# Optimization experiments

Hardware: AMD Instinct MI355X
Metric: run time of the kernel (lower is better)

The kernel has to match this reference:

```python
import jax, jax.numpy as jnp
import numpy as np

EPS = 1e-4


def setup_inputs() -> dict:
    key = jax.random.key(0)
    ks = jax.random.split(key, 16)
    N, D, H, K = 262144, 162, 256, 30
    s = 0.05  # weight init scale
    return {
        "Yh": jax.random.uniform(ks[0], (N, D), dtype=jnp.float32),
        "u": jax.random.uniform(ks[1], (1,), dtype=jnp.float32),
        "W1": jax.random.normal(ks[2], (D, H), dtype=jnp.float32) * s,
        "b1": jnp.zeros((H,), jnp.float32),
        "W2": jax.random.normal(ks[3], (H, H), dtype=jnp.float32) * s,
        "b2": jnp.zeros((H,), jnp.float32),
        "Wa": jax.random.normal(ks[4], (H, K), dtype=jnp.float32) * s,
        "ba": jnp.zeros((K,), jnp.float32),
        "Wb": jax.random.normal(ks[5], (H, K), dtype=jnp.float32) * s,
        "bb": jnp.zeros((K,), jnp.float32),
        "Wd1": jax.random.normal(ks[6], (K, H), dtype=jnp.float32) * s,
        "bd1": jnp.zeros((H,), jnp.float32),
        "Wd2": jax.random.normal(ks[7], (H, D), dtype=jnp.float32) * s,
        "bd2": jnp.zeros((D,), jnp.float32),
    }


def _stick_segments(v):
    # pi_k = v_k * prod_{j<k} (1 - v_j)  (vectorized exclusive cumprod,
    # replacing the original per-dim Python loop)
    cp = jnp.cumprod(1.0 - v, axis=1)  # [N, K]
    excl = jnp.concatenate([jnp.ones_like(v[:, :1]), cp[:, :-1]], axis=1)
    return v * excl


def reference(Yh, u, W1, b1, W2, b2, Wa, ba, Wb, bb, Wd1, bd1, Wd2, bd2):
    # encode_hsi: dense MLP -> positive Kumaraswamy params (softplus heads)
    h = jax.nn.relu(Yh @ W1 + b1)
    h = jax.nn.relu(h @ W2 + b2)
    alpha = jax.nn.softplus(h @ Wa + ba) + EPS  # param1_hsi [N, K]
    beta = jax.nn.softplus(h @ Wb + bb) + EPS   # param2_hsi [N, K]
    # Kumaraswamy reparametrization with a single shared uniform sample
    uu = u[0] * 0.98 + 0.01  # Uniform(0.01, 0.99) scalar
    v = (1.0 - uu ** (1.0 / beta)) ** (1.0 / alpha)  # [N, K]
    # set_v_K_to_one: force last stick proportion to 1
    v = jnp.concatenate([v[:, :-1], jnp.ones_like(v[:, :1])], axis=1)
    pi_h = _stick_segments(v)  # [N, K], rows sum to 1
    # decode: MLP -> sigmoid (positive outputs, recon.log() finite)
    d = jax.nn.relu(pi_h @ Wd1 + bd1)
    recon = jax.nn.sigmoid(d @ Wd2 + bd2)  # [N, D]
    return recon, alpha, beta, pi_h
```

## Files before the change

### kernel.cpp

```cpp
#include <hip/hip_runtime.h>
#include <hip/hip_bf16.h>

#define N_ROWS 262144
#define D_IN 162
#define K_DIM 30
#define ROWS 32

using bf16_t = __hip_bfloat16;
typedef __attribute__((ext_vector_type(8))) short bf16x8;
typedef __attribute__((ext_vector_type(4))) float f32x4;

__device__ __forceinline__ int swz_byte(int row, int col) {
  int b = (row << 9) + (col << 1);
  return b ^ ((row & 7) << 4);
}

__device__ __forceinline__ uint32_t bf16b(float x) {
  return (uint32_t)__builtin_bit_cast(unsigned short, __float2bfloat16(x));
}
__device__ __forceinline__ uint32_t pack2(float lo, float hi) {
  return bf16b(lo) | (bf16b(hi) << 16);
}
__device__ __forceinline__ float unpk_lo(uint32_t p) {
  return __bfloat162float(__builtin_bit_cast(__hip_bfloat16, (unsigned short)(p & 0xffff)));
}
__device__ __forceinline__ float unpk_hi(uint32_t p) {
  return __bfloat162float(__builtin_bit_cast(__hip_bfloat16, (unsigned short)(p >> 16)));
}
__device__ __forceinline__ float softplus_f(float x) {
  return (x > 15.f) ? x : log1pf(__expf(x));
}

__global__ void pack_b_kernel(const float* __restrict__ src, bf16_t* __restrict__ dst,
                              int K, int N, int Np, int KB) {
  int idx = blockIdx.x * 256 + threadIdx.x;
  int total = KB * Np * 32;
  if (idx >= total) return;
  int ks = idx & 31;
  int n  = (idx >> 5) % Np;
  int kb = idx / (32 * Np);
  int k  = kb * 32 + ks;
  float v = (k < K && n < N) ? src[k * N + n] : 0.f;
  dst[idx] = __float2bfloat16(v);
}

__global__ void pack_ab_kernel(const float* __restrict__ Wa, const float* __restrict__ Wb,
                               bf16_t* __restrict__ dst) {
  int idx = blockIdx.x * 256 + threadIdx.x;
  if (idx >= 8 * 64 * 32) return;
  int ks = idx & 31;
  int n  = (idx >> 5) & 63;
  int kb = idx >> 11;
  int k  = kb * 32 + ks;
  int j = n >> 1, s = n & 1;
  float v = (j < K_DIM) ? (s ? Wb[k * K_DIM + j] : Wa[k * K_DIM + j]) : 0.f;
  dst[idx] = __float2bfloat16(v);
}

template<int KB, int NP, int NMO>
__device__ __forceinline__ void gemm_acc(const uint8_t* lds, int srcOff,
                                         const bf16_t* __restrict__ Wp, int ocBase,
                                         int lr, int lg, f32x4 (&acc)[NMO][2]) {
  int bE[2], bO[2];
#pragma unroll
  for (int nr = 0; nr < 2; ++nr) {
    bE[nr] = srcOff + swz_byte(16 * nr + lr, 8 * lg);
    bO[nr] = srcOff + swz_byte(16 * nr + lr, 32 + 8 * lg);
  }
#pragma unroll
  for (int kb = 0; kb < KB; ++kb) {
    bf16x8 wf[NMO];
#pragma unroll
    for (int mo = 0; mo < NMO; ++mo)
      wf[mo] = *reinterpret_cast<const bf16x8*>(Wp + ((kb * NP + ocBase + 16 * mo + lr) << 5) + 8 * lg);
    bf16x8 hf[2];
#pragma unroll
    for (int nr = 0; nr < 2; ++nr) {
      int base = (kb & 1) ? bO[nr] : bE[nr];
      hf[nr] = *reinterpret_cast<const bf16x8*>(lds + base + (kb >> 1) * 128);
    }
#pragma unroll
    for (int mo = 0; mo < NMO; ++mo)
#pragma unroll
      for (int nr = 0; nr < 2; ++nr)
        acc[mo][nr] = __builtin_amdgcn_mfma_f32_16x16x32_bf16(wf[mo], hf[nr], acc[mo][nr], 0, 0, 0);
  }
}

template<int NMO>
__device__ __forceinline__ void acc_bias_init(const float* __restrict__ bias, int ocBase,
                                              int lg, f32x4 (&acc)[NMO][2]) {
#pragma unroll
  for (int mo = 0; mo < NMO; ++mo) {
    float4 bv = *reinterpret_cast<const float4*>(bias + ocBase + 16 * mo + 4 * lg);
    f32x4 t = {bv.x, bv.y, bv.z, bv.w};
#pragma unroll
    for (int nr = 0; nr < 2; ++nr) acc[mo][nr] = t;
  }
}

template<int NMO>
__device__ __forceinline__ void epi_relu_store(uint8_t* lds, int dstOff, int ocBase,
                                               int lr, int lg, f32x4 (&acc)[NMO][2]) {
#pragma unroll
  for (int mo = 0; mo < NMO; ++mo)
#pragma unroll
    for (int nr = 0; nr < 2; ++nr) {
      int row = 16 * nr + lr;
      int col = ocBase + 16 * mo + 4 * lg;
      float x0 = fmaxf(acc[mo][nr][0], 0.f), x1 = fmaxf(acc[mo][nr][1], 0.f);
      float x2 = fmaxf(acc[mo][nr][2], 0.f), x3 = fmaxf(acc[mo][nr][3], 0.f);
      uint2 p; p.x = pack2(x0, x1); p.y = pack2(x2, x3);
      *reinterpret_cast<uint2*>(lds + dstOff + swz_byte(row, col)) = p;
    }
}

#define OFF_H 16384
#define OFF_PI 8192
__launch_bounds__(256, 4)
__global__ void usdn_fused(const float* __restrict__ Yh, const float* __restrict__ u,
                           const float* __restrict__ b1, const float* __restrict__ b2,
                           const float* __restrict__ ba, const float* __restrict__ bb,
                           const float* __restrict__ bd1, const float* __restrict__ bd2,
                           const bf16_t* __restrict__ Wp1, const bf16_t* __restrict__ Wp2,
                           const bf16_t* __restrict__ Wpab, const bf16_t* __restrict__ Wpd1,
                           const bf16_t* __restrict__ Wpd2,
                           float* __restrict__ outRecon, float* __restrict__ outAlpha,
                           float* __restrict__ outBeta, float* __restrict__ outPi) {
  __shared__ __align__(16) uint8_t lds[32768];

  const int tid = threadIdx.x;
  const int w  = tid >> 6;
  const int l  = tid & 63;
  const int lr = l & 15;
  const int lg = l >> 4;
  const int r0 = blockIdx.x * ROWS;

  {
    int row = tid >> 3, l8 = tid & 7;
    const float2* src = reinterpret_cast<const float2*>(Yh + (size_t)(r0 + row) * D_IN);
#pragma unroll
    for (int it = 0; it < 12; ++it) {
      int f2 = l8 + it * 8;
      uint32_t p = 0;
      if (f2 < 81) { float2 v = src[f2]; p = pack2(v.x, v.y); }
      if (f2 < 96) *reinterpret_cast<uint32_t*>(lds + swz_byte(row, f2 * 2)) = p;
    }
  }
  __syncthreads();

  {
    f32x4 acc[4][2];
    acc_bias_init<4>(b1, w * 64, lg, acc);
    gemm_acc<6, 256, 4>(lds, 0, Wp1, w * 64, lr, lg, acc);
    epi_relu_store<4>(lds, OFF_H, w * 64, lr, lg, acc);
  }
  __syncthreads();

  {
    f32x4 acc[4][2];
    acc_bias_init<4>(b2, w * 64, lg, acc);
    gemm_acc<8, 256, 4>(lds, OFF_H, Wp2, w * 64, lr, lg, acc);
    __syncthreads();
    epi_relu_store<4>(lds, OFF_H, w * 64, lr, lg, acc);
  }
  __syncthreads();

  float regA0[2], regA1[2], regB0[2], regB1[2];
  int   j0 = 8 * w + 2 * lg;
  {
    bool jv = (j0 < K_DIM);
    float ba0 = jv ? ba[j0] : 0.f,     bb0 = jv ? bb[j0] : 0.f;
    float ba1 = jv ? ba[j0 + 1] : 0.f, bb1 = jv ? bb[j0 + 1] : 0.f;
    f32x4 acc[1][2];
    f32x4 binit = {ba0, bb0, ba1, bb1};
    acc[0][0] = binit; acc[0][1] = binit;
    gemm_acc<8, 64, 1>(lds, OFF_H, Wpab, 16 * w, lr, lg, acc);

    float uu  = u[0] * 0.98f + 0.01f;
    float l2u = log2f(uu);
    float* vbuf = reinterpret_cast<float*>(lds);
#pragma unroll
    for (int nr = 0; nr < 2; ++nr) {
      int row = 16 * nr + lr;
      float a0 = softplus_f(acc[0][nr][0]) + 1e-4f;
      float b0v = softplus_f(acc[0][nr][1]) + 1e-4f;
      float a1 = softplus_f(acc[0][nr][2]) + 1e-4f;
      float b1v = softplus_f(acc[0][nr][3]) + 1e-4f;
      regA0[nr] = a0; regB0[nr] = b0v; regA1[nr] = a1; regB1[nr] = b1v;
      if (jv) {
        if (j0 < K_DIM - 1) {
          float t = exp2f(l2u / b0v);
          vbuf[row * 33 + j0] = exp2f(log2f(1.f - t) / a0);
        }
        if (j0 + 1 < K_DIM - 1) {
          float t = exp2f(l2u / b1v);
          vbuf[row * 33 + j0 + 1] = exp2f(log2f(1.f - t) / a1);
        }
      }
    }
  }
  __syncthreads();

  if (tid < ROWS) {
    const float* vbuf = reinterpret_cast<const float*>(lds);
    bf16_t* piT = reinterpret_cast<bf16_t*>(lds + OFF_PI);
    int row = tid;
    float ex = 1.f;
#pragma unroll
    for (int j = 0; j < K_DIM - 1; ++j) {
      float vj = vbuf[row * 33 + j];
      float pi = vj * ex;
      piT[row * 40 + j] = __float2bfloat16(pi);
      ex *= (1.f - vj);
    }
    piT[row * 40 + (K_DIM - 1)] = __float2bfloat16(ex);
    piT[row * 40 + 30] = __float2bfloat16(0.f);
    piT[row * 40 + 31] = __float2bfloat16(0.f);
  }
  __syncthreads();

  {
    f32x4 acc[4][2];
    acc_bias_init<4>(bd1, w * 64, lg, acc);
    bf16x8 pf[2];
#pragma unroll
    for (int nr = 0; nr < 2; ++nr)
      pf[nr] = *reinterpret_cast<const bf16x8*>(lds + OFF_PI + (16 * nr + lr) * 80 + 16 * lg);
#pragma unroll
    for (int mo = 0; mo < 4; ++mo) {
      bf16x8 wf = *reinterpret_cast<const bf16x8*>(Wpd1 + ((w * 64 + 16 * mo + lr) << 5) + 8 * lg);
#pragma unroll
      for (int nr = 0; nr < 2; ++nr)
        acc[mo][nr] = __builtin_amdgcn_mfma_f32_16x16x32_bf16(wf, pf[nr], acc[mo][nr], 0, 0, 0);
    }
    epi_relu_store<4>(lds, OFF_H, w * 64, lr, lg, acc);
  }
  __syncthreads();

  {
    f32x4 acc[3][2];
#pragma unroll
    for (int mo = 0; mo < 3; ++mo) {
      int col0 = 48 * w + 16 * mo + 4 * lg;
      f32x4 t;
#pragma unroll
      for (int i = 0; i < 4; ++i) t[i] = (col0 + i < D_IN) ? bd2[col0 + i] : 0.f;
#pragma unroll
      for (int nr = 0; nr < 2; ++nr) acc[mo][nr] = t;
    }
    gemm_acc<8, 192, 3>(lds, OFF_H, Wpd2, 48 * w, lr, lg, acc);
#pragma unroll
    for (int mo = 0; mo < 3; ++mo) {
      int col0 = 48 * w + 16 * mo + 4 * lg;
#pragma unroll
      for (int nr = 0; nr < 2; ++nr) {
        int row = 16 * nr + lr;
        float s0 = 1.f / (1.f + __expf(-acc[mo][nr][0]));
        float s1 = 1.f / (1.f + __expf(-acc[mo][nr][1]));
        float s2 = 1.f / (1.f + __expf(-acc[mo][nr][2]));
        float s3 = 1.f / (1.f + __expf(-acc[mo][nr][3]));
        float* dst = outRecon + (size_t)(r0 + row) * D_IN + col0;
        if (col0 < D_IN)     *reinterpret_cast<float2*>(dst)     = make_float2(s0, s1);
        if (col0 + 2 < D_IN) *reinterpret_cast<float2*>(dst + 2) = make_float2(s2, s3);
      }
    }
  }

  if (j0 < K_DIM) {
#pragma unroll
    for (int nr = 0; nr < 2; ++nr) {
      int row = 16 * nr + lr;
      size_t base = (size_t)(r0 + row) * K_DIM + j0;
      *reinterpret_cast<float2*>(outAlpha + base) = make_float2(regA0[nr], regA1[nr]);
      *reinterpret_cast<float2*>(outBeta  + base) = make_float2(regB0[nr], regB1[nr]);
    }
  }
  {
    int row = tid >> 3, l8 = tid & 7;
#pragma unroll
    for (int half = 0; half < 2; ++half) {
      int f2 = l8 + half * 8;
      if (f2 < 15) {
        uint32_t pp = *reinterpret_cast<const uint32_t*>(lds + OFF_PI + row * 80 + f2 * 4);
        *reinterpret_cast<float2*>(outPi + (size_t)(r0 + row) * K_DIM + f2 * 2) =
            make_float2(unpk_lo(pp), unpk_hi(pp));
      }
    }
  }
}

extern "C" void kernel_launch(void* const* d_in, const int* in_sizes, int n_in,
                              void* d_out, int out_size, void* d_ws, size_t ws_size,
                              hipStream_t stream) {
  const float* Yh  = (const float*)d_in[0];
  const float* u   = (const float*)d_in[1];
  const float* W1  = (const float*)d_in[2];
  const float* b1  = (const float*)d_in[3];
  const float* W2  = (const float*)d_in[4];
  const float* b2  = (const float*)d_in[5];
  const float* Wa  = (const float*)d_in[6];
  const float* ba  = (const float*)d_in[7];
  const float* Wb  = (const float*)d_in[8];
  const float* bb  = (const float*)d_in[9];
  const float* Wd1 = (const float*)d_in[10];
  const float* bd1 = (const float*)d_in[11];
  const float* Wd2 = (const float*)d_in[12];
  const float* bd2 = (const float*)d_in[13];

  bf16_t* ws   = (bf16_t*)d_ws;
  bf16_t* Wp1  = ws;
  bf16_t* Wp2  = Wp1 + 49152;
  bf16_t* Wpab = Wp2 + 65536;
  bf16_t* Wpd1 = Wpab + 16384;
  bf16_t* Wpd2 = Wpd1 + 8192;

  float* outRecon = (float*)d_out;
  float* outAlpha = outRecon + (size_t)N_ROWS * D_IN;
  float* outBeta  = outAlpha + (size_t)N_ROWS * K_DIM;
  float* outPi    = outBeta  + (size_t)N_ROWS * K_DIM;

  pack_b_kernel<<<192, 256, 0, stream>>>(W1, Wp1, 162, 256, 256, 6);
  pack_b_kernel<<<256, 256, 0, stream>>>(W2, Wp2, 256, 256, 256, 8);
  pack_ab_kernel<<<64, 256, 0, stream>>>(Wa, Wb, Wpab);
  pack_b_kernel<<<32, 256, 0, stream>>>(Wd1, Wpd1, 30, 256, 256, 1);
  pack_b_kernel<<<192, 256, 0, stream>>>(Wd2, Wpd2, 256, 162, 192, 8);

  usdn_fused<<<N_ROWS / ROWS, 256, 0, stream>>>(Yh, u, b1, b2, ba, bb, bd1, bd2,
                                                Wp1, Wp2, Wpab, Wpd1, Wpd2,
                                                outRecon, outAlpha, outBeta, outPi);
}
```

Measured before the change: 280.7 us.

## Prefetch weight fragments across GEMM stages with double-buffered registers and ping-pong LDS

Weight fragments for each GEMM are now loaded two k-blocks ahead into a register double buffer, and the next stage's first fragments are issued before the current stage's epilogue. This is meant to hide global/L2 weight-load latency behind MFMA work. LDS buffers now alternate between two regions, which removes the intra-stage barrier before the layer-2 writeback. The cost is higher register pressure, which could cause spills or lower occupancy under launch_bounds(256,4).

```diff
diff --git a/kernel.cpp b/kernel.cpp
--- a/kernel.cpp
+++ b/kernel.cpp
@@ -57,10 +57,20 @@
   dst[idx] = __float2bfloat16(v);
 }
 
+template<int NP, int NMO>
+__device__ __forceinline__ void wload(const bf16_t* __restrict__ Wp, int kb, int ocBase,
+                                      int lr, int lg, bf16x8 (&out)[NMO]) {
+#pragma unroll
+  for (int mo = 0; mo < NMO; ++mo)
+    out[mo] = *reinterpret_cast<const bf16x8*>(
+        Wp + ((kb * NP + ocBase + 16 * mo + lr) << 5) + 8 * lg);
+}
+
 template<int KB, int NP, int NMO>
-__device__ __forceinline__ void gemm_acc(const uint8_t* lds, int srcOff,
-                                         const bf16_t* __restrict__ Wp, int ocBase,
-                                         int lr, int lg, f32x4 (&acc)[NMO][2]) {
+__device__ __forceinline__ void gemm_roll(const uint8_t* lds, int srcOff,
+                                          const bf16_t* __restrict__ Wp, int ocBase,
+                                          int lr, int lg, f32x4 (&acc)[NMO][2],
+                                          bf16x8 (&wbuf)[2][NMO]) {
   int bE[2], bO[2];
 #pragma unroll
   for (int nr = 0; nr < 2; ++nr) {
@@ -69,10 +79,11 @@
   }
 #pragma unroll
   for (int kb = 0; kb < KB; ++kb) {
-    bf16x8 wf[NMO];
-#pragma unroll
-    for (int mo = 0; mo < NMO; ++mo)
-      wf[mo] = *reinterpret_cast<const bf16x8*>(Wp + ((kb * NP + ocBase + 16 * mo + lr) << 5) + 8 * lg);
+    bf16x8 cur[NMO];
+#pragma unroll
+    for (int mo = 0; mo < NMO; ++mo) cur[mo] = wbuf[kb & 1][mo];
+    if (kb + 2 < KB)
+      wload<NP, NMO>(Wp, kb + 2, ocBase, lr, lg, wbuf[kb & 1]);
     bf16x8 hf[2];
 #pragma unroll
     for (int nr = 0; nr < 2; ++nr) {
@@ -83,7 +94,7 @@
     for (int mo = 0; mo < NMO; ++mo)
 #pragma unroll
       for (int nr = 0; nr < 2; ++nr)
-        acc[mo][nr] = __builtin_amdgcn_mfma_f32_16x16x32_bf16(wf[mo], hf[nr], acc[mo][nr], 0, 0, 0);
+        acc[mo][nr] = __builtin_amdgcn_mfma_f32_16x16x32_bf16(cur[mo], hf[nr], acc[mo][nr], 0, 0, 0);
   }
 }
 
@@ -115,8 +126,9 @@
     }
 }
 
-#define OFF_H 16384
-#define OFF_PI 8192
+#define OFF_B  16384
+#define OFF_PI (16384 + 8192)
+
 __launch_bounds__(256, 4)
 __global__ void usdn_fused(const float* __restrict__ Yh, const float* __restrict__ u,
                            const float* __restrict__ b1, const float* __restrict__ b2,
@@ -136,57 +148,93 @@
   const int lg = l >> 4;
   const int r0 = blockIdx.x * ROWS;
 
-  {
-    int row = tid >> 3, l8 = tid & 7;
-    const float2* src = reinterpret_cast<const float2*>(Yh + (size_t)(r0 + row) * D_IN);
+  const int srow = tid >> 3, sl8 = tid & 7;
+  float2 sv[12];
+  {
+    const float2* src = reinterpret_cast<const float2*>(Yh + (size_t)(r0 + srow) * D_IN);
 #pragma unroll
     for (int it = 0; it < 12; ++it) {
-      int f2 = l8 + it * 8;
+      int f2 = sl8 + it * 8;
+      if (f2 < 81) sv[it] = src[f2];
+    }
+  }
+  bf16x8 w1buf[2][4];
+  wload<256, 4>(Wp1, 0, w * 64, lr, lg, w1buf[0]);
+  wload<256, 4>(Wp1, 1, w * 64, lr, lg, w1buf[1]);
+  {
+#pragma unroll
+    for (int it = 0; it < 12; ++it) {
+      int f2 = sl8 + it * 8;
       uint32_t p = 0;
-      if (f2 < 81) { float2 v = src[f2]; p = pack2(v.x, v.y); }
-      if (f2 < 96) *reinterpret_cast<uint32_t*>(lds + swz_byte(row, f2 * 2)) = p;
-    }
-  }
-  __syncthreads();
-
+      if (f2 < 81) p = pack2(sv[it].x, sv[it].y);
+      if (f2 < 96) *reinterpret_cast<uint32_t*>(lds + swz_byte(srow, f2 * 2)) = p;
+    }
+  }
+  __syncthreads();
+
+  bf16x8 w2buf[2][4];
   {
     f32x4 acc[4][2];
     acc_bias_init<4>(b1, w * 64, lg, acc);
-    gemm_acc<6, 256, 4>(lds, 0, Wp1, w * 64, lr, lg, acc);
-    epi_relu_store<4>(lds, OFF_H, w * 64, lr, lg, acc);
-  }
-  __syncthreads();
-
+    gemm_roll<6, 256, 4>(lds, 0, Wp1, w * 64, lr, lg, acc, w1buf);
+    wload<256, 4>(Wp2, 0, w * 64, lr, lg, w2buf[0]);
+    wload<256, 4>(Wp2, 1, w * 64, lr, lg, w2buf[1]);
+    epi_relu_store<4>(lds, OFF_B, w * 64, lr, lg, acc);
+  }
+  __syncthreads();
+
+  bf16x8 wh[8];
   {
     f32x4 acc[4][2];
     acc_bias_init<4>(b2, w * 64, lg, acc);
-    gemm_acc<8, 256, 4>(lds, OFF_H, Wp2, w * 64, lr, lg, acc);
-    __syncthreads();
-    epi_relu_store<4>(lds, OFF_H, w * 64, lr, lg, acc);
+    gemm_roll<8, 256, 4>(lds, OFF_B, Wp2, w * 64, lr, lg, acc, w2buf);
+#pragma unroll
+    for (int kb = 0; kb < 8; ++kb)
+      wh[kb] = *reinterpret_cast<const bf16x8*>(Wpab + ((kb * 64 + 16 * w + lr) << 5) + 8 * lg);
+    epi_relu_store<4>(lds, 0, w * 64, lr, lg, acc);
   }
   __syncthreads();
 
   float regA0[2], regA1[2], regB0[2], regB1[2];
-  int   j0 = 8 * w + 2 * lg;
+  const int j0 = 8 * w + 2 * lg;
+  bf16x8 w4[4];
+  bf16x8 w5buf[2][3];
   {
     bool jv = (j0 < K_DIM);
     float ba0 = jv ? ba[j0] : 0.f,     bb0 = jv ? bb[j0] : 0.f;
     float ba1 = jv ? ba[j0 + 1] : 0.f, bb1 = jv ? bb[j0 + 1] : 0.f;
-    f32x4 acc[1][2];
+    f32x4 acc[2];
     f32x4 binit = {ba0, bb0, ba1, bb1};
-    acc[0][0] = binit; acc[0][1] = binit;
-    gemm_acc<8, 64, 1>(lds, OFF_H, Wpab, 16 * w, lr, lg, acc);
+    acc[0] = binit; acc[1] = binit;
+    int bE[2], bO[2];
+#pragma unroll
+    for (int nr = 0; nr < 2; ++nr) {
+      bE[nr] = swz_byte(16 * nr + lr, 8 * lg);
+      bO[nr] = swz_byte(16 * nr + lr, 32 + 8 * lg);
+    }
+#pragma unroll
+    for (int kb = 0; kb < 8; ++kb) {
+#pragma unroll
+      for (int nr = 0; nr < 2; ++nr) {
+        int base = (kb & 1) ? bO[nr] : bE[nr];
+        bf16x8 hf = *reinterpret_cast<const bf16x8*>(lds + base + (kb >> 1) * 128);
+        acc[nr] = __builtin_amdgcn_mfma_f32_16x16x32_bf16(wh[kb], hf, acc[nr], 0, 0, 0);
+      }
+    }
+    wload<256, 4>(Wpd1, 0, w * 64, lr, lg, w4);
+    wload<192, 3>(Wpd2, 0, 48 * w, lr, lg, w5buf[0]);
+    wload<192, 3>(Wpd2, 1, 48 * w, lr, lg, w5buf[1]);
 
     float uu  = u[0] * 0.98f + 0.01f;
     float l2u = log2f(uu);
-    float* vbuf = reinterpret_cast<float*>(lds);
+    float* vbuf = reinterpret_cast<float*>(lds + OFF_B);
 #pragma unroll
     for (int nr = 0; nr < 2; ++nr) {
       int row = 16 * nr + lr;
-      float a0 = softplus_f(acc[0][nr][0]) + 1e-4f;
-      float b0v = softplus_f(acc[0][nr][1]) + 1e-4f;
-      float a1 = softplus_f(acc[0][nr][2]) + 1e-4f;
-      float b1v = softplus_f(acc[0][nr][3]) + 1e-4f;
+      float a0  = softplus_f(acc[nr][0]) + 1e-4f;
+      float b0v = softplus_f(acc[nr][1]) + 1e-4f;
+      float a1  = softplus_f(acc[nr][2]) + 1e-4f;
+      float b1v = softplus_f(acc[nr][3]) + 1e-4f;
       regA0[nr] = a0; regB0[nr] = b0v; regA1[nr] = a1; regB1[nr] = b1v;
       if (jv) {
         if (j0 < K_DIM - 1) {
@@ -203,7 +251,7 @@
   __syncthreads();
 
   if (tid < ROWS) {
-    const float* vbuf = reinterpret_cast<const float*>(lds);
+    const float* vbuf = reinterpret_cast<const float*>(lds + OFF_B);
     bf16_t* piT = reinterpret_cast<bf16_t*>(lds + OFF_PI);
     int row = tid;
     float ex = 1.f;
@@ -228,13 +276,11 @@
     for (int nr = 0; nr < 2; ++nr)
       pf[nr] = *reinterpret_cast<const bf16x8*>(lds + OFF_PI + (16 * nr + lr) * 80 + 16 * lg);
 #pragma unroll
-    for (int mo = 0; mo < 4; ++mo) {
-      bf16x8 wf = *reinterpret_cast<const bf16x8*>(Wpd1 + ((w * 64 + 16 * mo + lr) << 5) + 8 * lg);
+    for (int mo = 0; mo < 4; ++mo)
 #pragma unroll
       for (int nr = 0; nr < 2; ++nr)
-        acc[mo][nr] = __builtin_amdgcn_mfma_f32_16x16x32_bf16(wf, pf[nr], acc[mo][nr], 0, 0, 0);
-    }
-    epi_relu_store<4>(lds, OFF_H, w * 64, lr, lg, acc);
+        acc[mo][nr] = __builtin_amdgcn_mfma_f32_16x16x32_bf16(w4[mo], pf[nr], acc[mo][nr], 0, 0, 0);
+    epi_relu_store<4>(lds, 0, w * 64, lr, lg, acc);
   }
   __syncthreads();
 
@@ -249,7 +295,7 @@
 #pragma unroll
       for (int nr = 0; nr < 2; ++nr) acc[mo][nr] = t;
     }
-    gemm_acc<8, 192, 3>(lds, OFF_H, Wpd2, 48 * w, lr, lg, acc);
+    gemm_roll<8, 192, 3>(lds, 0, Wpd2, 48 * w, lr, lg, acc, w5buf);
 #pragma unroll
     for (int mo = 0; mo < 3; ++mo) {
       int col0 = 48 * w + 16 * mo + 4 * lg;
```

Result: faster. 269.9 us (-3.9%).
